# Optimization experiments

Measured on AMD Instinct MI355X. Metric: run time of the kernel, lower is better.

## Reference

```python
import jax, jax.numpy as jnp
import numpy as np

B, T, F = 2048, 24, 16
N = 65536
D = T * F


def setup_inputs() -> dict:
    key = jax.random.key(0)
    k1, k2, k3 = jax.random.split(key, 3)
    x = jax.random.normal(k1, (B, T, F), dtype=jnp.float32)
    X_train = jax.random.normal(k2, (N, D), dtype=jnp.float32)
    Y_train = jax.random.normal(k3, (N, 24, 1), dtype=jnp.float32)
    return {"x": x, "X_train": X_train, "Y_train": Y_train}


def reference(x, X_train, Y_train):
    x_flat = x.reshape(x.shape[0], -1)  # [B, D]
    # Euclidean cdist via ||a||^2 + ||b||^2 - 2 a.b (GEMM-dominated)
    xx = jnp.sum(x_flat * x_flat, axis=1, keepdims=True)       # [B, 1]
    tt = jnp.sum(X_train * X_train, axis=1)[None, :]           # [1, N]
    cross = x_flat @ X_train.T                                  # [B, N]
    d2 = jnp.maximum(xx + tt - 2.0 * cross, 0.0)
    distances = jnp.sqrt(d2)                                    # [B, N]
    nearest = jnp.argmin(distances, axis=1)                     # [B]
    y_pred = Y_train[nearest]                                   # [B, 24, 1]
    return y_pred
```

## Files before the change

kernel.cpp:

```cpp
#include <hip/hip_runtime.h>
#include <cfloat>

#define B_Q 2048
#define N_T 65536
#define DIM 384

typedef __attribute__((ext_vector_type(8))) _Float16 f16x8;
typedef __attribute__((ext_vector_type(4))) float f32x4;

__device__ __forceinline__ void gload16(const void* g, void* l) {
  __builtin_amdgcn_global_load_lds(
      (const __attribute__((address_space(1))) void*)g,
      (__attribute__((address_space(3))) void*)l, 16, 0, 0);
}

__global__ void split_kernel(const float* __restrict__ in, _Float16* __restrict__ hi,
                             _Float16* __restrict__ lo, int n8) {
  int i = blockIdx.x * 256 + threadIdx.x;
  if (i >= n8) return;
  float4 a = ((const float4*)in)[2 * i];
  float4 b = ((const float4*)in)[2 * i + 1];
  float v[8] = {a.x, a.y, a.z, a.w, b.x, b.y, b.z, b.w};
  f16x8 h, l;
#pragma unroll
  for (int j = 0; j < 8; ++j) {
    _Float16 hj = (_Float16)v[j];
    h[j] = hj;
    l[j] = (_Float16)(v[j] - (float)hj);
  }
  *(f16x8*)(hi + 8 * (size_t)i) = h;
  *(f16x8*)(lo + 8 * (size_t)i) = l;
}

__global__ void tt_kernel(const float* __restrict__ Xt, float* __restrict__ tt) {
  const int wave = threadIdx.x >> 6;
  const int lane = threadIdx.x & 63;
  const int row = blockIdx.x * 4 + wave;
  const float* p = Xt + (size_t)row * DIM;
  float s = 0.f;
#pragma unroll
  for (int i = 0; i < DIM / 64; ++i) {
    float v = p[lane + 64 * i];
    s = fmaf(v, v, s);
  }
#pragma unroll
  for (int off = 32; off > 0; off >>= 1) s += __shfl_xor(s, off, 64);
  if (lane == 0) tt[row] = s;
}

__global__ __launch_bounds__(256, 2) void dist_mfma(
    const _Float16* __restrict__ xh, const _Float16* __restrict__ xl,
    const _Float16* __restrict__ th, const _Float16* __restrict__ tl,
    const float* __restrict__ tt, float* __restrict__ pval, int* __restrict__ pidx) {
  __shared__ _Float16 Ah[128][32];
  __shared__ _Float16 Al[128][32];
  __shared__ _Float16 Bh[128][32];
  __shared__ _Float16 Bl[128][32];

  const int t = threadIdx.x;
  const int lane = t & 63;
  const int wid = t >> 6;
  const int wm = wid >> 1, wn = wid & 1;
  const int r15 = lane & 15, g = lane >> 4;
  const int qbase = blockIdx.x * 128;
  const int strip = blockIdx.y;

  const int srow = t >> 2;
  const int schunk = t & 3;
  const size_t aoff0 = (size_t)(qbase + srow) * DIM + schunk * 8;
  const size_t aoff1 = aoff0 + (size_t)64 * DIM;
  char* ldsA = (char*)&Ah[0][0] + t * 16;
  char* ldsAl = (char*)&Al[0][0] + t * 16;
  char* ldsB = (char*)&Bh[0][0] + t * 16;
  char* ldsBl = (char*)&Bl[0][0] + t * 16;

  float bestv[4][4];
  int besti[4][4];
#pragma unroll
  for (int mf = 0; mf < 4; ++mf)
#pragma unroll
    for (int j = 0; j < 4; ++j) { bestv[mf][j] = FLT_MAX; besti[mf][j] = 0x7fffffff; }

  for (int tile = 0; tile < 8; ++tile) {
    const int nbase = strip * 1024 + tile * 128;
    const size_t boff0 = (size_t)(nbase + srow) * DIM + schunk * 8;
    const size_t boff1 = boff0 + (size_t)64 * DIM;

    f32x4 acc[4][4];
#pragma unroll
    for (int mf = 0; mf < 4; ++mf)
#pragma unroll
      for (int nf = 0; nf < 4; ++nf) acc[mf][nf] = (f32x4){0.f, 0.f, 0.f, 0.f};

    for (int kt = 0; kt < DIM / 32; ++kt) {
      const int ko = kt * 32;
      __syncthreads();
      gload16(xh + aoff0 + ko, ldsA);
      gload16(xh + aoff1 + ko, ldsA + 4096);
      gload16(xl + aoff0 + ko, ldsAl);
      gload16(xl + aoff1 + ko, ldsAl + 4096);
      gload16(th + boff0 + ko, ldsB);
      gload16(th + boff1 + ko, ldsB + 4096);
      gload16(tl + boff0 + ko, ldsBl);
      gload16(tl + boff1 + ko, ldsBl + 4096);
      __syncthreads();

      const _Float16* pA = &Ah[wm * 64 + r15][g * 8];
      const _Float16* pAl = &Al[wm * 64 + r15][g * 8];
      const _Float16* pB = &Bh[wn * 64 + r15][g * 8];
      const _Float16* pBl = &Bl[wn * 64 + r15][g * 8];
      f16x8 a_h[4], a_l[4];
#pragma unroll
      for (int mf = 0; mf < 4; ++mf) {
        a_h[mf] = *(const f16x8*)(pA + mf * 512);
        a_l[mf] = *(const f16x8*)(pAl + mf * 512);
      }
#pragma unroll
      for (int nf = 0; nf < 4; ++nf) {
        f16x8 b_h = *(const f16x8*)(pB + nf * 512);
        f16x8 b_l = *(const f16x8*)(pBl + nf * 512);
#pragma unroll
        for (int mf = 0; mf < 4; ++mf) {
          acc[mf][nf] = __builtin_amdgcn_mfma_f32_16x16x32_f16(a_h[mf], b_h, acc[mf][nf], 0, 0, 0);
          acc[mf][nf] = __builtin_amdgcn_mfma_f32_16x16x32_f16(a_h[mf], b_l, acc[mf][nf], 0, 0, 0);
          acc[mf][nf] = __builtin_amdgcn_mfma_f32_16x16x32_f16(a_l[mf], b_h, acc[mf][nf], 0, 0, 0);
        }
      }
    }

    int ncol[4];
    float ttv[4];
#pragma unroll
    for (int nf = 0; nf < 4; ++nf) {
      ncol[nf] = nbase + wn * 64 + nf * 16 + r15;
      ttv[nf] = tt[ncol[nf]];
    }
#pragma unroll
    for (int mf = 0; mf < 4; ++mf)
#pragma unroll
      for (int nf = 0; nf < 4; ++nf)
#pragma unroll
        for (int j = 0; j < 4; ++j) {
          float s = fmaf(-2.f, acc[mf][nf][j], ttv[nf]);
          if (s < bestv[mf][j] || (s == bestv[mf][j] && ncol[nf] < besti[mf][j])) {
            bestv[mf][j] = s;
            besti[mf][j] = ncol[nf];
          }
        }
  }

#pragma unroll
  for (int mf = 0; mf < 4; ++mf)
#pragma unroll
    for (int j = 0; j < 4; ++j) {
      float v = bestv[mf][j];
      int ix = besti[mf][j];
#pragma unroll
      for (int off = 1; off < 16; off <<= 1) {
        float ov = __shfl_xor(v, off, 64);
        int oi = __shfl_xor(ix, off, 64);
        if (ov < v || (ov == v && oi < ix)) { v = ov; ix = oi; }
      }
      if (r15 == 0) {
        int m = qbase + wm * 64 + mf * 16 + g * 4 + j;
        pval[(size_t)m * 128 + strip * 2 + wn] = v;
        pidx[(size_t)m * 128 + strip * 2 + wn] = ix;
      }
    }
}

__global__ void reduce128(const float* __restrict__ pval, const int* __restrict__ pidx,
                          const float* __restrict__ Y, float* __restrict__ out) {
  const int wid = threadIdx.x >> 6;
  const int lane = threadIdx.x & 63;
  const int q = blockIdx.x * 4 + wid;
  float v = pval[(size_t)q * 128 + lane];
  int ix = pidx[(size_t)q * 128 + lane];
  float v1 = pval[(size_t)q * 128 + 64 + lane];
  int i1 = pidx[(size_t)q * 128 + 64 + lane];
  if (v1 < v || (v1 == v && i1 < ix)) { v = v1; ix = i1; }
#pragma unroll
  for (int off = 32; off > 0; off >>= 1) {
    float ov = __shfl_xor(v, off, 64);
    int oi = __shfl_xor(ix, off, 64);
    if (ov < v || (ov == v && oi < ix)) { v = ov; ix = oi; }
  }
  if (lane < 24) out[(size_t)q * 24 + lane] = Y[(size_t)ix * 24 + lane];
}

#define BK 16
#define PAD 132
__global__ __launch_bounds__(256) void dist_f32(
    const float* __restrict__ x, const float* __restrict__ Xt,
    const float* __restrict__ tt, float* __restrict__ pval, int* __restrict__ pidx) {
  __shared__ float As[BK][PAD];
  __shared__ float Bs[BK][PAD];
  const int t = threadIdx.x;
  const int tx = t & 15;
  const int ty = t >> 4;
  const int qbase = blockIdx.x * 128;
  const int strip = blockIdx.y;
  float bestv[8];
  int besti[8];
#pragma unroll
  for (int i = 0; i < 8; ++i) { bestv[i] = FLT_MAX; besti[i] = 0x7fffffff; }
  for (int tile = 0; tile < 8; ++tile) {
    const int nbase = strip * 1024 + tile * 128;
    float acc[8][8];
#pragma unroll
    for (int i = 0; i < 8; ++i)
#pragma unroll
      for (int j = 0; j < 8; ++j) acc[i][j] = 0.f;
    for (int kt = 0; kt < DIM / BK; ++kt) {
      const int kbase = kt * BK;
      __syncthreads();
#pragma unroll
      for (int it = 0; it < 2; ++it) {
        int idx = t + it * 256;
        int row = idx >> 2;
        int k4 = (idx & 3) << 2;
        float4 va = *(const float4*)(x + (size_t)(qbase + row) * DIM + kbase + k4);
        As[k4 + 0][row] = va.x; As[k4 + 1][row] = va.y;
        As[k4 + 2][row] = va.z; As[k4 + 3][row] = va.w;
        float4 vb = *(const float4*)(Xt + (size_t)(nbase + row) * DIM + kbase + k4);
        Bs[k4 + 0][row] = vb.x; Bs[k4 + 1][row] = vb.y;
        Bs[k4 + 2][row] = vb.z; Bs[k4 + 3][row] = vb.w;
      }
      __syncthreads();
#pragma unroll
      for (int kk = 0; kk < BK; ++kk) {
        float4 a0 = *(const float4*)&As[kk][ty * 4];
        float4 a1 = *(const float4*)&As[kk][64 + ty * 4];
        float4 b0 = *(const float4*)&Bs[kk][tx * 4];
        float4 b1 = *(const float4*)&Bs[kk][64 + tx * 4];
        float a[8] = {a0.x, a0.y, a0.z, a0.w, a1.x, a1.y, a1.z, a1.w};
        float b[8] = {b0.x, b0.y, b0.z, b0.w, b1.x, b1.y, b1.z, b1.w};
#pragma unroll
        for (int i = 0; i < 8; ++i)
#pragma unroll
          for (int j = 0; j < 8; ++j) acc[i][j] = fmaf(a[i], b[j], acc[i][j]);
      }
    }
    int cols[8];
    float ttv[8];
#pragma unroll
    for (int j = 0; j < 8; ++j) {
      cols[j] = nbase + (j < 4 ? tx * 4 + j : 64 + tx * 4 + (j - 4));
      ttv[j] = tt[cols[j]];
    }
#pragma unroll
    for (int i = 0; i < 8; ++i)
#pragma unroll
      for (int j = 0; j < 8; ++j) {
        float s = fmaf(-2.f, acc[i][j], ttv[j]);
        if (s < bestv[i] || (s == bestv[i] && cols[j] < besti[i])) {
          bestv[i] = s; besti[i] = cols[j];
        }
      }
  }
#pragma unroll
  for (int i = 0; i < 8; ++i) {
    float v = bestv[i];
    int ix = besti[i];
#pragma unroll
    for (int off = 1; off < 16; off <<= 1) {
      float ov = __shfl_xor(v, off, 64);
      int oi = __shfl_xor(ix, off, 64);
      if (ov < v || (ov == v && oi < ix)) { v = ov; ix = oi; }
    }
    if (tx == 0) {
      int row = qbase + (i < 4 ? ty * 4 + i : 64 + ty * 4 + (i - 4));
      pval[(size_t)row * 64 + strip] = v;
      pidx[(size_t)row * 64 + strip] = ix;
    }
  }
}

__global__ void reduce64(const float* __restrict__ pval, const int* __restrict__ pidx,
                         const float* __restrict__ Y, float* __restrict__ out) {
  const int wid = threadIdx.x >> 6;
  const int lane = threadIdx.x & 63;
  const int q = blockIdx.x * 4 + wid;
  float v = pval[(size_t)q * 64 + lane];
  int ix = pidx[(size_t)q * 64 + lane];
#pragma unroll
  for (int off = 32; off > 0; off >>= 1) {
    float ov = __shfl_xor(v, off, 64);
    int oi = __shfl_xor(ix, off, 64);
    if (ov < v || (ov == v && oi < ix)) { v = ov; ix = oi; }
  }
  if (lane < 24) out[(size_t)q * 24 + lane] = Y[(size_t)ix * 24 + lane];
}

extern "C" void kernel_launch(void* const* d_in, const int* in_sizes, int n_in,
                              void* d_out, int out_size, void* d_ws, size_t ws_size,
                              hipStream_t stream) {
  const float* x  = (const float*)d_in[0];
  const float* Xt = (const float*)d_in[1];
  const float* Y  = (const float*)d_in[2];
  float* out = (float*)d_out;

  _Float16* th = (_Float16*)d_ws;
  _Float16* tl = th + (size_t)N_T * DIM;
  _Float16* xh = tl + (size_t)N_T * DIM;
  _Float16* xl = xh + (size_t)B_Q * DIM;
  float* tt = (float*)(xl + (size_t)B_Q * DIM);
  float* pval = tt + N_T;
  int* pidx = (int*)(pval + (size_t)B_Q * 128);
  size_t need = (size_t)((char*)(pidx + (size_t)B_Q * 128) - (char*)d_ws);

  if (ws_size >= need) {
    split_kernel<<<(N_T * DIM / 8 + 255) / 256, 256, 0, stream>>>(Xt, th, tl, N_T * DIM / 8);
    split_kernel<<<(B_Q * DIM / 8 + 255) / 256, 256, 0, stream>>>(x, xh, xl, B_Q * DIM / 8);
    tt_kernel<<<N_T / 4, 256, 0, stream>>>(Xt, tt);
    dist_mfma<<<dim3(B_Q / 128, 64), 256, 0, stream>>>(xh, xl, th, tl, tt, pval, pidx);
    reduce128<<<B_Q / 4, 256, 0, stream>>>(pval, pidx, Y, out);
  } else {
    float* tt2 = (float*)d_ws;
    float* pv2 = tt2 + N_T;
    int* pi2 = (int*)(pv2 + (size_t)B_Q * 64);
    tt_kernel<<<N_T / 4, 256, 0, stream>>>(Xt, tt2);
    dist_f32<<<dim3(B_Q / 128, 64), 256, 0, stream>>>(x, Xt, tt2, pv2, pi2);
    reduce64<<<B_Q / 4, 256, 0, stream>>>(pv2, pi2, Y, out);
  }
}
```

Measured before the change: 514.1 us.

## Enlarge MFMA distance tiles with register-staged prefetch and swizzled LDS

```diff
diff --git a/kernel.cpp b/kernel.cpp
--- a/kernel.cpp
+++ b/kernel.cpp
@@ -4,15 +4,13 @@
 #define B_Q 2048
 #define N_T 65536
 #define DIM 384
+#define NSTRIPS 32
+#define TILES 8
+#define KSTEPS 12
+#define TOTAL_STEPS (TILES * KSTEPS)
 
 typedef __attribute__((ext_vector_type(8))) _Float16 f16x8;
 typedef __attribute__((ext_vector_type(4))) float f32x4;
-
-__device__ __forceinline__ void gload16(const void* g, void* l) {
-  __builtin_amdgcn_global_load_lds(
-      (const __attribute__((address_space(1))) void*)g,
-      (__attribute__((address_space(3))) void*)l, 16, 0, 0);
-}
 
 __global__ void split_kernel(const float* __restrict__ in, _Float16* __restrict__ hi,
                              _Float16* __restrict__ lo, int n8) {
@@ -48,137 +46,149 @@
   if (lane == 0) tt[row] = s;
 }
 
-__global__ __launch_bounds__(256, 2) void dist_mfma(
+__global__ __launch_bounds__(512, 2) void dist_mfma2(
     const _Float16* __restrict__ xh, const _Float16* __restrict__ xl,
     const _Float16* __restrict__ th, const _Float16* __restrict__ tl,
     const float* __restrict__ tt, float* __restrict__ pval, int* __restrict__ pidx) {
-  __shared__ _Float16 Ah[128][32];
-  __shared__ _Float16 Al[128][32];
-  __shared__ _Float16 Bh[128][32];
-  __shared__ _Float16 Bl[128][32];
+  __shared__ __align__(16) char SM[65536];
+  const int AH = 0, AL = 16384, BH = 32768, BL = 49152;
 
   const int t = threadIdx.x;
   const int lane = t & 63;
   const int wid = t >> 6;
   const int wm = wid >> 1, wn = wid & 1;
   const int r15 = lane & 15, g = lane >> 4;
-  const int qbase = blockIdx.x * 128;
-  const int strip = blockIdx.y;
-
-  const int srow = t >> 2;
-  const int schunk = t & 3;
-  const size_t aoff0 = (size_t)(qbase + srow) * DIM + schunk * 8;
-  const size_t aoff1 = aoff0 + (size_t)64 * DIM;
-  char* ldsA = (char*)&Ah[0][0] + t * 16;
-  char* ldsAl = (char*)&Al[0][0] + t * 16;
-  char* ldsB = (char*)&Bh[0][0] + t * 16;
-  char* ldsBl = (char*)&Bl[0][0] + t * 16;
-
-  float bestv[4][4];
-  int besti[4][4];
+  const int qbase = blockIdx.y * 256;
+  const int strip = blockIdx.x;
+
+  const int r0 = t >> 2, ch = t & 3;
+  const int sch = ch ^ ((r0 >> 1) & 3);
+  const int wo = r0 * 64 + sch * 16;
+  const size_t aoff = (size_t)(qbase + r0) * DIM + ch * 8;
+  const size_t boff = (size_t)(strip * 2048 + r0) * DIM + ch * 8;
+
+  f16x8 sreg[8];
+  auto stage_load = [&](int step) {
+    int tile = step / KSTEPS;
+    int kt = step - tile * KSTEPS;
+    size_t a0 = aoff + kt * 32;
+    size_t b0 = boff + (size_t)tile * (256 * DIM) + kt * 32;
+    sreg[0] = *(const f16x8*)(xh + a0);
+    sreg[1] = *(const f16x8*)(xh + a0 + (size_t)128 * DIM);
+    sreg[2] = *(const f16x8*)(xl + a0);
+    sreg[3] = *(const f16x8*)(xl + a0 + (size_t)128 * DIM);
+    sreg[4] = *(const f16x8*)(th + b0);
+    sreg[5] = *(const f16x8*)(th + b0 + (size_t)128 * DIM);
+    sreg[6] = *(const f16x8*)(tl + b0);
+    sreg[7] = *(const f16x8*)(tl + b0 + (size_t)128 * DIM);
+  };
+  auto stage_write = [&]() {
+    *(f16x8*)(SM + AH + wo) = sreg[0];
+    *(f16x8*)(SM + AH + wo + 8192) = sreg[1];
+    *(f16x8*)(SM + AL + wo) = sreg[2];
+    *(f16x8*)(SM + AL + wo + 8192) = sreg[3];
+    *(f16x8*)(SM + BH + wo) = sreg[4];
+    *(f16x8*)(SM + BH + wo + 8192) = sreg[5];
+    *(f16x8*)(SM + BL + wo) = sreg[6];
+    *(f16x8*)(SM + BL + wo + 8192) = sreg[7];
+  };
+  auto frag = [&](int base, int row, int gg) -> f16x8 {
+    int off = base + row * 64 + ((gg ^ ((row >> 1) & 3)) << 4);
+    return *(const f16x8*)(SM + off);
+  };
+
+  f32x4 acc[4][8];
 #pragma unroll
   for (int mf = 0; mf < 4; ++mf)
 #pragma unroll
-    for (int j = 0; j < 4; ++j) { bestv[mf][j] = FLT_MAX; besti[mf][j] = 0x7fffffff; }
-
-  for (int tile = 0; tile < 8; ++tile) {
-    const int nbase = strip * 1024 + tile * 128;
-    const size_t boff0 = (size_t)(nbase + srow) * DIM + schunk * 8;
-    const size_t boff1 = boff0 + (size_t)64 * DIM;
-
-    f32x4 acc[4][4];
-#pragma unroll
-    for (int mf = 0; mf < 4; ++mf)
-#pragma unroll
-      for (int nf = 0; nf < 4; ++nf) acc[mf][nf] = (f32x4){0.f, 0.f, 0.f, 0.f};
-
-    for (int kt = 0; kt < DIM / 32; ++kt) {
-      const int ko = kt * 32;
-      __syncthreads();
-      gload16(xh + aoff0 + ko, ldsA);
-      gload16(xh + aoff1 + ko, ldsA + 4096);
-      gload16(xl + aoff0 + ko, ldsAl);
-      gload16(xl + aoff1 + ko, ldsAl + 4096);
-      gload16(th + boff0 + ko, ldsB);
-      gload16(th + boff1 + ko, ldsB + 4096);
-      gload16(tl + boff0 + ko, ldsBl);
-      gload16(tl + boff1 + ko, ldsBl + 4096);
-      __syncthreads();
-
-      const _Float16* pA = &Ah[wm * 64 + r15][g * 8];
-      const _Float16* pAl = &Al[wm * 64 + r15][g * 8];
-      const _Float16* pB = &Bh[wn * 64 + r15][g * 8];
-      const _Float16* pBl = &Bl[wn * 64 + r15][g * 8];
-      f16x8 a_h[4], a_l[4];
+    for (int nf = 0; nf < 8; ++nf) acc[mf][nf] = (f32x4){0.f, 0.f, 0.f, 0.f};
+
+  float bestv = FLT_MAX;
+  int besti = 0x7fffffff;
+
+  stage_load(0);
+  stage_write();
+  __syncthreads();
+
+  for (int step = 0; step < TOTAL_STEPS; ++step) {
+    const int tile = step / KSTEPS;
+    const int kt = step - tile * KSTEPS;
+    const bool has_next = (step + 1 < TOTAL_STEPS);
+    if (has_next) stage_load(step + 1);
+
+    f16x8 ah[4], al[4];
+#pragma unroll
+    for (int mf = 0; mf < 4; ++mf) {
+      int row = wm * 64 + mf * 16 + r15;
+      ah[mf] = frag(AH, row, g);
+      al[mf] = frag(AL, row, g);
+    }
+#pragma unroll
+    for (int nf = 0; nf < 8; ++nf) {
+      int row = wn * 128 + nf * 16 + r15;
+      f16x8 bh = frag(BH, row, g);
+      f16x8 bl = frag(BL, row, g);
 #pragma unroll
       for (int mf = 0; mf < 4; ++mf) {
-        a_h[mf] = *(const f16x8*)(pA + mf * 512);
-        a_l[mf] = *(const f16x8*)(pAl + mf * 512);
+        acc[mf][nf] = __builtin_amdgcn_mfma_f32_16x16x32_f16(ah[mf], bh, acc[mf][nf], 0, 0, 0);
+        acc[mf][nf] = __builtin_amdgcn_mfma_f32_16x16x32_f16(ah[mf], bl, acc[mf][nf], 0, 0, 0);
+        acc[mf][nf] = __builtin_amdgcn_mfma_f32_16x16x32_f16(al[mf], bh, acc[mf][nf], 0, 0, 0);
       }
-#pragma unroll
-      for (int nf = 0; nf < 4; ++nf) {
-        f16x8 b_h = *(const f16x8*)(pB + nf * 512);
-        f16x8 b_l = *(const f16x8*)(pBl + nf * 512);
-#pragma unroll
-        for (int mf = 0; mf < 4; ++mf) {
-          acc[mf][nf] = __builtin_amdgcn_mfma_f32_16x16x32_f16(a_h[mf], b_h, acc[mf][nf], 0, 0, 0);
-          acc[mf][nf] = __builtin_amdgcn_mfma_f32_16x16x32_f16(a_h[mf], b_l, acc[mf][nf], 0, 0, 0);
-          acc[mf][nf] = __builtin_amdgcn_mfma_f32_16x16x32_f16(a_l[mf], b_h, acc[mf][nf], 0, 0, 0);
-        }
-      }
-    }
-
-    int ncol[4];
-    float ttv[4];
-#pragma unroll
-    for (int nf = 0; nf < 4; ++nf) {
-      ncol[nf] = nbase + wn * 64 + nf * 16 + r15;
-      ttv[nf] = tt[ncol[nf]];
-    }
-#pragma unroll
-    for (int mf = 0; mf < 4; ++mf)
-#pragma unroll
-      for (int nf = 0; nf < 4; ++nf)
+    }
+
+    if (kt == KSTEPS - 1) {
+      const int nb = strip * 2048 + tile * 256;
+      float ttv[8];
+#pragma unroll
+      for (int nf = 0; nf < 8; ++nf) ttv[nf] = tt[nb + wn * 128 + nf * 16 + r15];
+#pragma unroll
+      for (int mf = 0; mf < 4; ++mf)
 #pragma unroll
         for (int j = 0; j < 4; ++j) {
-          float s = fmaf(-2.f, acc[mf][nf][j], ttv[nf]);
-          if (s < bestv[mf][j] || (s == bestv[mf][j] && ncol[nf] < besti[mf][j])) {
-            bestv[mf][j] = s;
-            besti[mf][j] = ncol[nf];
+          float v = fmaf(-2.f, acc[mf][0][j], ttv[0]);
+          int ix = nb + wn * 128 + r15;
+#pragma unroll
+          for (int nf = 1; nf < 8; ++nf) {
+            float s = fmaf(-2.f, acc[mf][nf][j], ttv[nf]);
+            if (s < v) { v = s; ix = nb + wn * 128 + nf * 16 + r15; }
+          }
+#pragma unroll
+          for (int off = 1; off < 16; off <<= 1) {
+            float ov = __shfl_xor(v, off, 64);
+            int oi = __shfl_xor(ix, off, 64);
+            if (ov < v || (ov == v && oi < ix)) { v = ov; ix = oi; }
+          }
+          float rv = __shfl(v, ((lane >> 2) & 3) << 4, 64);
+          int ri = __shfl(ix, ((lane >> 2) & 3) << 4, 64);
+          if ((lane >> 4) == mf && (lane & 3) == j) {
+            if (rv < bestv || (rv == bestv && ri < besti)) { bestv = rv; besti = ri; }
           }
         }
-  }
-
-#pragma unroll
-  for (int mf = 0; mf < 4; ++mf)
-#pragma unroll
-    for (int j = 0; j < 4; ++j) {
-      float v = bestv[mf][j];
-      int ix = besti[mf][j];
-#pragma unroll
-      for (int off = 1; off < 16; off <<= 1) {
-        float ov = __shfl_xor(v, off, 64);
-        int oi = __shfl_xor(ix, off, 64);
-        if (ov < v || (ov == v && oi < ix)) { v = ov; ix = oi; }
-      }
-      if (r15 == 0) {
-        int m = qbase + wm * 64 + mf * 16 + g * 4 + j;
-        pval[(size_t)m * 128 + strip * 2 + wn] = v;
-        pidx[(size_t)m * 128 + strip * 2 + wn] = ix;
-      }
-    }
-}
-
-__global__ void reduce128(const float* __restrict__ pval, const int* __restrict__ pidx,
-                          const float* __restrict__ Y, float* __restrict__ out) {
+#pragma unroll
+      for (int mf = 0; mf < 4; ++mf)
+#pragma unroll
+        for (int nf = 0; nf < 8; ++nf) acc[mf][nf] = (f32x4){0.f, 0.f, 0.f, 0.f};
+    }
+
+    __syncthreads();
+    if (has_next) {
+      stage_write();
+      __syncthreads();
+    }
+  }
+
+  const int q = qbase + wm * 64 + lane;
+  pval[(size_t)q * 64 + strip * 2 + wn] = bestv;
+  pidx[(size_t)q * 64 + strip * 2 + wn] = besti;
+}
+
+__global__ void reduce64(const float* __restrict__ pval, const int* __restrict__ pidx,
+                         const float* __restrict__ Y, float* __restrict__ out) {
   const int wid = threadIdx.x >> 6;
   const int lane = threadIdx.x & 63;
   const int q = blockIdx.x * 4 + wid;
-  float v = pval[(size_t)q * 128 + lane];
-  int ix = pidx[(size_t)q * 128 + lane];
-  float v1 = pval[(size_t)q * 128 + 64 + lane];
-  int i1 = pidx[(size_t)q * 128 + 64 + lane];
-  if (v1 < v || (v1 == v && i1 < ix)) { v = v1; ix = i1; }
+  float v = pval[(size_t)q * 64 + lane];
+  int ix = pidx[(size_t)q * 64 + lane];
 #pragma unroll
   for (int off = 32; off > 0; off >>= 1) {
     float ov = __shfl_xor(v, off, 64);
@@ -276,22 +286,6 @@
   }
 }
 
-__global__ void reduce64(const float* __restrict__ pval, const int* __restrict__ pidx,
-                         const float* __restrict__ Y, float* __restrict__ out) {
-  const int wid = threadIdx.x >> 6;
-  const int lane = threadIdx.x & 63;
-  const int q = blockIdx.x * 4 + wid;
-  float v = pval[(size_t)q * 64 + lane];
-  int ix = pidx[(size_t)q * 64 + lane];
-#pragma unroll
-  for (int off = 32; off > 0; off >>= 1) {
-    float ov = __shfl_xor(v, off, 64);
-    int oi = __shfl_xor(ix, off, 64);
-    if (ov < v || (ov == v && oi < ix)) { v = ov; ix = oi; }
-  }
-  if (lane < 24) out[(size_t)q * 24 + lane] = Y[(size_t)ix * 24 + lane];
-}
-
 extern "C" void kernel_launch(void* const* d_in, const int* in_sizes, int n_in,
                               void* d_out, int out_size, void* d_ws, size_t ws_size,
                               hipStream_t stream) {
@@ -306,15 +300,15 @@
   _Float16* xl = xh + (size_t)B_Q * DIM;
   float* tt = (float*)(xl + (size_t)B_Q * DIM);
   float* pval = tt + N_T;
-  int* pidx = (int*)(pval + (size_t)B_Q * 128);
-  size_t need = (size_t)((char*)(pidx + (size_t)B_Q * 128) - (char*)d_ws);
+  int* pidx = (int*)(pval + (size_t)B_Q * 64);
+  size_t need = (size_t)((char*)(pidx + (size_t)B_Q * 64) - (char*)d_ws);
 
   if (ws_size >= need) {
     split_kernel<<<(N_T * DIM / 8 + 255) / 256, 256, 0, stream>>>(Xt, th, tl, N_T * DIM / 8);
     split_kernel<<<(B_Q * DIM / 8 + 255) / 256, 256, 0, stream>>>(x, xh, xl, B_Q * DIM / 8);
     tt_kernel<<<N_T / 4, 256, 0, stream>>>(Xt, tt);
-    dist_mfma<<<dim3(B_Q / 128, 64), 256, 0, stream>>>(xh, xl, th, tl, tt, pval, pidx);
-    reduce128<<<B_Q / 4, 256, 0, stream>>>(pval, pidx, Y, out);
+    dist_mfma2<<<dim3(NSTRIPS, B_Q / 256), 512, 0, stream>>>(xh, xl, th, tl, tt, pval, pidx);
+    reduce64<<<B_Q / 4, 256, 0, stream>>>(pval, pidx, Y, out);
   } else {
     float* tt2 = (float*)d_ws;
     float* pv2 = tt2 + N_T;
```

Measured after the change: 484.8 us. 1.06x faster.
